# Kernel optimization log

Measured on AMD Instinct MI355X. Metric: run time of the kernel, lower is better.

The kernel has to match this reference:

```python
import jax, jax.numpy as jnp
import numpy as np

B, S, E, H = 2, 2048, 1024, 16
D = E // H  # head_dim = 64


def setup_inputs() -> dict:
    key = jax.random.key(0)
    k1, k2, k3 = jax.random.split(key, 3)
    scale = 0.02  # GPT-2 init scale
    return {
        "hidden_states": jax.random.normal(k1, (B, S, E), dtype=jnp.float32),
        "c_attn_w": jax.random.normal(k2, (E, 3 * E), dtype=jnp.float32) * scale,
        "c_attn_b": jnp.zeros((3 * E,), dtype=jnp.float32),
        "c_proj_w": jax.random.normal(k3, (E, E), dtype=jnp.float32) * scale,
        "c_proj_b": jnp.zeros((E,), dtype=jnp.float32),
    }


def reference(hidden_states, c_attn_w, c_attn_b, c_proj_w, c_proj_b):
    # Conv1D: x @ W + b  -> qkv [B, S, 3E]
    qkv = hidden_states @ c_attn_w + c_attn_b
    q, k, v = jnp.split(qkv, 3, axis=-1)

    # split heads -> [B, H, S, D]
    def split_heads(t):
        return t.reshape(B, S, H, D).transpose(0, 2, 1, 3)

    q, k, v = split_heads(q), split_heads(k), split_heads(v)

    # naive full attention: QK^T / sqrt(D) -> softmax -> @ V
    attn_weights = jnp.einsum("bhqd,bhkd->bhqk", q, k) / jnp.sqrt(
        jnp.asarray(D, dtype=q.dtype)
    )
    attn_weights = jax.nn.softmax(attn_weights, axis=-1)
    attn_output = jnp.einsum("bhqk,bhkd->bhqd", attn_weights, v)

    # merge heads -> [B, S, E], then output projection
    attn_output = attn_output.transpose(0, 2, 1, 3).reshape(B, S, E)
    attn_output = attn_output @ c_proj_w + c_proj_b
    return attn_output
```

## Files before the change

kernel.cpp:

```cpp
#include <hip/hip_runtime.h>

#define SEQ 2048
#define EMB 1024
#define KDIM 1024
#define CF 0.180336880111113f

typedef __attribute__((ext_vector_type(8))) short short8_t;
typedef __attribute__((ext_vector_type(4))) float floatx4;
typedef __attribute__((ext_vector_type(4))) unsigned short ushort4_t;
typedef __attribute__((ext_vector_type(4))) unsigned int uivec4;

#define GLOAD16(gp, lp)                                                        \
  __builtin_amdgcn_global_load_lds(                                            \
      (const __attribute__((address_space(1))) void*)(gp),                     \
      (__attribute__((address_space(3))) void*)(lp), 16, 0, 0)

#define WGBAR()                                   \
  do {                                            \
    __asm__ __volatile__("" ::: "memory");        \
    __builtin_amdgcn_s_barrier();                 \
    __asm__ __volatile__("" ::: "memory");        \
  } while (0)

static __device__ __forceinline__ unsigned short f2bf(float x) {
  unsigned int u = __float_as_uint(x);
  return (unsigned short)((u + 0x7fffu + ((u >> 16) & 1u)) >> 16);
}

static __device__ __forceinline__ short8_t mk_pb(unsigned int a, unsigned int b,
                                                 unsigned int c, unsigned int d) {
  uivec4 t;
  t[0] = a; t[1] = b; t[2] = c; t[3] = d;
  return __builtin_bit_cast(short8_t, t);
}

static __device__ __forceinline__ unsigned int pack_bf(float p0, float p1) {
  return __builtin_amdgcn_perm(__float_as_uint(p1), __float_as_uint(p0),
                               0x07060302u);
}

static __device__ __forceinline__ void tconv_tile(
    const float* __restrict__ W, unsigned short* __restrict__ T, int N, int K,
    int n0, int k0, int tid) {
  __shared__ float Tl[64][65];
  const int lx = tid & 15, ly = tid >> 4;
#pragma unroll
  for (int u = 0; u < 4; ++u) {
    int r = u * 16 + ly;
    float4 v = *(const float4*)&W[(size_t)(k0 + r) * N + n0 + lx * 4];
    Tl[r][lx * 4 + 0] = v.x;
    Tl[r][lx * 4 + 1] = v.y;
    Tl[r][lx * 4 + 2] = v.z;
    Tl[r][lx * 4 + 3] = v.w;
  }
  __syncthreads();
#pragma unroll
  for (int u = 0; u < 4; ++u) {
    int n = u * 16 + ly;
    ushort4_t h;
#pragma unroll
    for (int v = 0; v < 4; ++v) h[v] = f2bf(Tl[lx * 4 + v][n]);
    *(ushort4_t*)&T[(size_t)(n0 + n) * K + k0 + lx * 4] = h;
  }
}

__global__ __launch_bounds__(256) void prep(
    const float* __restrict__ hs, const float* __restrict__ caw,
    const float* __restrict__ cpw, unsigned short* __restrict__ hsb,
    unsigned short* __restrict__ w1t, unsigned short* __restrict__ w2t) {
  const int bid = blockIdx.x, tid = threadIdx.x;
  if (bid < 4096) {
    const int i = bid * 256 + tid;
    float4 v = *(const float4*)&hs[(size_t)i * 4];
    ushort4_t h = {f2bf(v.x), f2bf(v.y), f2bf(v.z), f2bf(v.w)};
    *(ushort4_t*)&hsb[(size_t)i * 4] = h;
  } else if (bid < 4864) {
    const int idx = bid - 4096;
    tconv_tile(caw, w1t, 3 * EMB, EMB, (idx % 48) * 64, (idx / 48) * 64, tid);
  } else {
    const int idx = bid - 4864;
    tconv_tile(cpw, w2t, EMB, EMB, (idx % 16) * 64, (idx / 16) * 64, tid);
  }
}

template <int MODE, int BN>
__global__ __launch_bounds__(256) void gemm_pl(
    const unsigned short* __restrict__ Ag, const unsigned short* __restrict__ Bg,
    const float* __restrict__ bias, float* __restrict__ outF,
    unsigned short* __restrict__ qk, unsigned short* __restrict__ vt) {
  __shared__ __attribute__((aligned(16))) unsigned short Ah[3][128 * 32];
  __shared__ __attribute__((aligned(16))) unsigned short Bh[3][BN * 32];
  const int NJ = BN / 32;

  const int tid = threadIdx.x;
  const int w = tid >> 6, lane = tid & 63;
  const int quad = lane >> 4, c = lane & 15;

  int bm, bn;
  {
    const int L = blockIdx.x, x = L & 7, g = L >> 3;
    if (MODE == 0) {
      bm = ((x & 1) * 16 + (g & 15)) * 128;
      bn = ((x >> 1) * 6 + (g >> 4)) * 128;
    } else {
      bm = ((x & 3) * 8 + (g & 7)) * 128;
      bn = ((x >> 2) * 8 + (g >> 3)) * 64;
    }
  }
  const int wm = (w >> 1) * 64, wn = (w & 1) * (BN / 2);

  const unsigned short* gsrc = (w < 2) ? Ag : Bg;
  const int lbo = (w < 2) ? (w & 1) * 64 * 32 : (w & 1) * (BN / 2) * 32;
  const int rbase = (w < 2) ? (bm + (w & 1) * 64) : (bn + (w & 1) * (BN / 2));
  const int nloads = (w < 2) ? 4 : (BN / 32);
  const int srow = lane >> 2;
  const int sblk = (lane & 3) ^ ((lane >> 3) & 3);
  const char* gp0 = (const char*)(gsrc + (size_t)(rbase + srow) * KDIM) + sblk * 16;

  floatx4 acc[4][NJ];
  const floatx4 z = {0.f, 0.f, 0.f, 0.f};
#pragma unroll
  for (int i = 0; i < 4; ++i)
#pragma unroll
    for (int j = 0; j < NJ; ++j) acc[i][j] = z;

  const int sw = (c >> 1) & 3;

#define STAGE_G(buf, kt)                                                       \
  do {                                                                         \
    unsigned short* ld = ((w < 2) ? Ah[buf] : Bh[buf]) + lbo;                  \
    const char* gp = gp0 + (size_t)(kt) * 64;                                  \
    for (int i_ = 0; i_ < nloads; ++i_)                                        \
      GLOAD16(gp + (size_t)i_ * 16 * (KDIM * 2), &ld[i_ * 512]);               \
  } while (0)

  STAGE_G(0, 0);
  STAGE_G(1, 1);

  for (int t = 0; t < 32; ++t) {
    if (BN == 128 || w < 2) {
      __asm__ __volatile__("s_waitcnt vmcnt(4)" ::: "memory");
    } else {
      __asm__ __volatile__("s_waitcnt vmcnt(2)" ::: "memory");
    }
    WGBAR();
    STAGE_G((t + 2) % 3, (t + 2) & 31);
    const unsigned short* Ac = Ah[t % 3];
    const unsigned short* Bc = Bh[t % 3];

    const int oct = (quad ^ sw) * 8;
    short8_t a[4], b[NJ];
#pragma unroll
    for (int i = 0; i < 4; ++i)
      a[i] = *(const short8_t*)&Ac[(wm + 16 * i + c) * 32 + oct];
#pragma unroll
    for (int j = 0; j < NJ; ++j)
      b[j] = *(const short8_t*)&Bc[(wn + 16 * j + c) * 32 + oct];
#pragma unroll
    for (int i = 0; i < 4; ++i)
#pragma unroll
      for (int j = 0; j < NJ; ++j)
        acc[i][j] = __builtin_amdgcn_mfma_f32_16x16x32_bf16(b[j], a[i], acc[i][j], 0, 0, 0);
  }
#undef STAGE_G

  __asm__ __volatile__("s_waitcnt vmcnt(0)" ::: "memory");

#pragma unroll
  for (int i = 0; i < 4; ++i) {
    const int row = bm + wm + 16 * i + c;
#pragma unroll
    for (int j = 0; j < NJ; ++j) {
      const int col0 = bn + wn + 16 * j + quad * 4;
      floatx4 v = acc[i][j] + *(const floatx4*)&bias[col0];
      if (MODE == 0) {
        if (col0 < 1024) v = v * CF;
        if (col0 < 2048) {
          ushort4_t pk = {f2bf(v[0]), f2bf(v[1]), f2bf(v[2]), f2bf(v[3])};
          *(ushort4_t*)&qk[(size_t)row * 2048 + col0] = pk;
        } else {
          const int c2 = col0 - 2048, hh = c2 >> 6, d0 = c2 & 63;
          const int bb = row >> 11, s = row & 2047;
          const int j = s & 63;
          const int lam = (j & 0x20) | ((j & 0x0C) << 1) | ((j & 0x10) >> 2) | (j & 3);
          const int sp = (s & ~63) | lam;
          unsigned short* vb = &vt[((size_t)(bb * 16 + hh) * 64 + d0) * 2048 + sp];
          vb[0 * 2048] = f2bf(v[0]);
          vb[1 * 2048] = f2bf(v[1]);
          vb[2 * 2048] = f2bf(v[2]);
          vb[3 * 2048] = f2bf(v[3]);
        }
      } else {
        *(floatx4*)&outF[(size_t)row * 1024 + col0] = v;
      }
    }
  }
}

static __device__ __forceinline__ void stage_kv(
    int w, int srow, int sblkg, const unsigned short* __restrict__ gK,
    const unsigned short* __restrict__ gV, unsigned short* Kbuf,
    unsigned short* Vbuf, int jt) {
  if (w < 2) {
    const unsigned short* g0 = gK + (size_t)(jt * 64 + w * 32 + srow) * 2048 + sblkg * 8;
    unsigned short* l0 = &Kbuf[(w * 32) * 64];
#pragma unroll
    for (int i = 0; i < 4; ++i) GLOAD16(g0 + (size_t)i * 8 * 2048, &l0[i * 512]);
  } else {
    const unsigned short* g0 = gV + (size_t)((w - 2) * 32 + srow) * 2048 + jt * 64 + sblkg * 8;
    unsigned short* l0 = &Vbuf[((w - 2) * 32) * 64];
#pragma unroll
    for (int i = 0; i < 4; ++i) GLOAD16(g0 + (size_t)i * 8 * 2048, &l0[i * 512]);
  }
}

__global__ __launch_bounds__(256, 4) void attn8(
    const unsigned short* __restrict__ qk, const unsigned short* __restrict__ vt,
    unsigned short* __restrict__ ao) {
  __shared__ __attribute__((aligned(16))) unsigned short SMEM[4 * 4096];
  unsigned short* Ksb = SMEM;
  unsigned short* Vsb = SMEM + 2 * 4096;

  const int tid = threadIdx.x;
  const int w = tid >> 6, lane = tid & 63, quad = lane >> 4, c = lane & 15;
  const int qh = w >> 1, kh = w & 1;
  const int L = blockIdx.x, x = L & 7, g = L >> 3;
  const int hb = x * 4 + (g >> 5);
  const int h = hb & 15, b = hb >> 4;
  const int q0 = (g & 31) * 64;
  const int rk = c & 7;

  short8_t qf[2][2];
  {
    const size_t rb = (size_t)b * SEQ + q0 + qh * 32;
#pragma unroll
    for (int mi = 0; mi < 2; ++mi) {
      const size_t qr = (rb + mi * 16 + c) * 2048 + h * 64 + quad * 8;
      qf[mi][0] = *(const short8_t*)&qk[qr];
      qf[mi][1] = *(const short8_t*)&qk[qr + 32];
    }
  }
  __asm__ __volatile__("s_waitcnt vmcnt(0)" ::: "memory");

  floatx4 O[2][4], Osum[2];
  const floatx4 z = {0.f, 0.f, 0.f, 0.f};
#pragma unroll
  for (int mi = 0; mi < 2; ++mi) {
    Osum[mi] = z;
#pragma unroll
    for (int dg = 0; dg < 4; ++dg) O[mi][dg] = z;
  }
  short8_t ones;
#pragma unroll
  for (int e = 0; e < 8; ++e) ones[e] = (short)0x3F80;

  const int srow = lane >> 3;
  const int sblkg = (lane & 7) ^ srow;
  const unsigned short* gK = qk + (size_t)b * SEQ * 2048 + 1024 + h * 64;
  const unsigned short* gV = vt + (size_t)(b * 16 + h) * 64 * 2048;

  stage_kv(w, srow, sblkg, gK, gV, Ksb, Vsb, 0);

  for (int t = 0; t < 32; ++t) {
    __asm__ __volatile__("s_waitcnt vmcnt(0)" ::: "memory");
    WGBAR();
    if (t < 31)
      stage_kv(w, srow, sblkg, gK, gV, Ksb + ((t + 1) & 1) * 4096,
               Vsb + ((t + 1) & 1) * 4096, t + 1);
    const unsigned short* Kc = Ksb + (t & 1) * 4096;
    const unsigned short* Vc = Vsb + (t & 1) * 4096;

    floatx4 S[2][2];
#pragma unroll
    for (int mi = 0; mi < 2; ++mi)
#pragma unroll
      for (int jg = 0; jg < 2; ++jg) S[mi][jg] = z;
#pragma unroll
    for (int kd = 0; kd < 2; ++kd) {
      const int oct = ((4 * kd + quad) ^ rk) * 8;
#pragma unroll
      for (int jg = 0; jg < 2; ++jg) {
        short8_t kf = *(const short8_t*)&Kc[((kh * 2 + jg) * 16 + c) * 64 + oct];
#pragma unroll
        for (int mi = 0; mi < 2; ++mi)
          S[mi][jg] = __builtin_amdgcn_mfma_f32_16x16x32_bf16(kf, qf[mi][kd], S[mi][jg], 0, 0, 0);
      }
    }

    unsigned int pw[2][2][2];
#pragma unroll
    for (int mi = 0; mi < 2; ++mi)
#pragma unroll
      for (int jg = 0; jg < 2; ++jg) {
        float p0 = __builtin_amdgcn_exp2f(S[mi][jg][0]);
        float p1 = __builtin_amdgcn_exp2f(S[mi][jg][1]);
        float p2 = __builtin_amdgcn_exp2f(S[mi][jg][2]);
        float p3 = __builtin_amdgcn_exp2f(S[mi][jg][3]);
        pw[mi][jg][0] = pack_bf(p0, p1);
        pw[mi][jg][1] = pack_bf(p2, p3);
      }

    const int octv = ((4 * kh + quad) ^ rk) * 8;
    short8_t pb[2];
#pragma unroll
    for (int mi = 0; mi < 2; ++mi) {
      pb[mi] = mk_pb(pw[mi][0][0], pw[mi][0][1], pw[mi][1][0], pw[mi][1][1]);
      Osum[mi] = __builtin_amdgcn_mfma_f32_16x16x32_bf16(ones, pb[mi], Osum[mi], 0, 0, 0);
    }
#pragma unroll
    for (int dg = 0; dg < 4; ++dg) {
      short8_t vf = *(const short8_t*)&Vc[(dg * 16 + c) * 64 + octv];
#pragma unroll
      for (int mi = 0; mi < 2; ++mi)
        O[mi][dg] = __builtin_amdgcn_mfma_f32_16x16x32_bf16(vf, pb[mi], O[mi][dg], 0, 0, 0);
    }
  }

  __asm__ __volatile__("s_waitcnt vmcnt(0)" ::: "memory");
  WGBAR();

  float* Of = (float*)SMEM;
  float* Ss = (float*)((char*)SMEM + 17408);
  if (kh == 1) {
#pragma unroll
    for (int mi = 0; mi < 2; ++mi) {
      const int row = mi * 16 + c;
      float* orow = &Of[(qh * 32 + row) * 68];
#pragma unroll
      for (int dg = 0; dg < 4; ++dg)
        *(floatx4*)&orow[dg * 16 + quad * 4] = O[mi][dg];
      if (quad == 0) Ss[qh * 32 + row] = Osum[mi][0];
    }
  }
  WGBAR();
  if (kh == 0) {
#pragma unroll
    for (int mi = 0; mi < 2; ++mi) {
      const int row = mi * 16 + c;
      const float inv = 1.0f / (Osum[mi][0] + Ss[qh * 32 + row]);
      const float* orow = &Of[(qh * 32 + row) * 68];
      const size_t grow = (size_t)b * SEQ + q0 + qh * 32 + row;
#pragma unroll
      for (int dg = 0; dg < 4; ++dg) {
        floatx4 o = O[mi][dg] + *(const floatx4*)&orow[dg * 16 + quad * 4];
        ushort4_t ov = {f2bf(o[0] * inv), f2bf(o[1] * inv),
                        f2bf(o[2] * inv), f2bf(o[3] * inv)};
        *(ushort4_t*)&ao[grow * EMB + h * 64 + dg * 16 + quad * 4] = ov;
      }
    }
  }
}

extern "C" void kernel_launch(void* const* d_in, const int* in_sizes, int n_in,
                              void* d_out, int out_size, void* d_ws, size_t ws_size,
                              hipStream_t stream) {
  const float* hs = (const float*)d_in[0];
  const float* c_attn_w = (const float*)d_in[1];
  const float* c_attn_b = (const float*)d_in[2];
  const float* c_proj_w = (const float*)d_in[3];
  const float* c_proj_b = (const float*)d_in[4];
  float* out = (float*)d_out;

  char* ws = (char*)d_ws;
  unsigned short* hsb = (unsigned short*)(ws + 0);
  unsigned short* qk  = (unsigned short*)(ws + 8388608);
  unsigned short* vt  = (unsigned short*)(ws + 25165824);
  unsigned short* aob = (unsigned short*)(ws + 33554432);
  unsigned short* w1t = (unsigned short*)(ws + 41943040);
  unsigned short* w2t = (unsigned short*)(ws + 48234496);

  prep<<<5120, 256, 0, stream>>>(hs, c_attn_w, c_proj_w, hsb, w1t, w2t);
  gemm_pl<0, 128><<<768, 256, 0, stream>>>(hsb, w1t, c_attn_b, nullptr, qk, vt);
  attn8<<<1024, 256, 0, stream>>>(qk, vt, aob);
  gemm_pl<2, 64><<<512, 256, 0, stream>>>(aob, w2t, c_proj_b, out, nullptr, nullptr);
}
```

Baseline: 176.9 us.

## Software-pipeline PV matmul one tile behind QK with triple-buffered V

Restructures the attention loop so the P·V and rowsum MFMAs for tile t-1 run after the QK^T MFMAs for tile t, which hides the exp/pack latency behind independent matrix work. V moves to a triple-buffered shared-memory ring, growing LDS to 40KB, so the previous tile's V stays valid while the next tile is staged. It also raises wave priority around the MFMA section with s_setprio. This adds register pressure from carrying pbPrev across iterations and needs an epilogue to drain the last tile.

```diff
diff --git a/kernel.cpp b/kernel.cpp
--- a/kernel.cpp
+++ b/kernel.cpp
@@ -214,10 +214,10 @@
   }
 }
 
-__global__ __launch_bounds__(256, 4) void attn8(
+__global__ __launch_bounds__(256, 4) void attn9(
     const unsigned short* __restrict__ qk, const unsigned short* __restrict__ vt,
     unsigned short* __restrict__ ao) {
-  __shared__ __attribute__((aligned(16))) unsigned short SMEM[4 * 4096];
+  __shared__ __attribute__((aligned(16))) unsigned short SMEM[5 * 4096];
   unsigned short* Ksb = SMEM;
   unsigned short* Vsb = SMEM + 2 * 4096;
 
@@ -259,6 +259,9 @@
   const unsigned short* gK = qk + (size_t)b * SEQ * 2048 + 1024 + h * 64;
   const unsigned short* gV = vt + (size_t)(b * 16 + h) * 64 * 2048;
 
+  const int octv = ((4 * kh + quad) ^ rk) * 8;
+  short8_t pbPrev[2];
+
   stage_kv(w, srow, sblkg, gK, gV, Ksb, Vsb, 0);
 
   for (int t = 0; t < 32; ++t) {
@@ -266,10 +269,10 @@
     WGBAR();
     if (t < 31)
       stage_kv(w, srow, sblkg, gK, gV, Ksb + ((t + 1) & 1) * 4096,
-               Vsb + ((t + 1) & 1) * 4096, t + 1);
+               Vsb + ((t + 1) % 3) * 4096, t + 1);
     const unsigned short* Kc = Ksb + (t & 1) * 4096;
-    const unsigned short* Vc = Vsb + (t & 1) * 4096;
-
+
+    __builtin_amdgcn_s_setprio(1);
     floatx4 S[2][2];
 #pragma unroll
     for (int mi = 0; mi < 2; ++mi)
@@ -287,36 +290,51 @@
       }
     }
 
-    unsigned int pw[2][2][2];
-#pragma unroll
-    for (int mi = 0; mi < 2; ++mi)
+    if (t != 0) {
+      const unsigned short* Vp = Vsb + ((t + 2) % 3) * 4096;
+#pragma unroll
+      for (int mi = 0; mi < 2; ++mi)
+        Osum[mi] = __builtin_amdgcn_mfma_f32_16x16x32_bf16(ones, pbPrev[mi], Osum[mi], 0, 0, 0);
+#pragma unroll
+      for (int dg = 0; dg < 4; ++dg) {
+        short8_t vf = *(const short8_t*)&Vp[(dg * 16 + c) * 64 + octv];
+#pragma unroll
+        for (int mi = 0; mi < 2; ++mi)
+          O[mi][dg] = __builtin_amdgcn_mfma_f32_16x16x32_bf16(vf, pbPrev[mi], O[mi][dg], 0, 0, 0);
+      }
+    }
+    __builtin_amdgcn_s_setprio(0);
+
+#pragma unroll
+    for (int mi = 0; mi < 2; ++mi) {
+      unsigned int pw[2][2];
 #pragma unroll
       for (int jg = 0; jg < 2; ++jg) {
         float p0 = __builtin_amdgcn_exp2f(S[mi][jg][0]);
         float p1 = __builtin_amdgcn_exp2f(S[mi][jg][1]);
         float p2 = __builtin_amdgcn_exp2f(S[mi][jg][2]);
         float p3 = __builtin_amdgcn_exp2f(S[mi][jg][3]);
-        pw[mi][jg][0] = pack_bf(p0, p1);
-        pw[mi][jg][1] = pack_bf(p2, p3);
-      }
-
-    const int octv = ((4 * kh + quad) ^ rk) * 8;
-    short8_t pb[2];
-#pragma unroll
-    for (int mi = 0; mi < 2; ++mi) {
-      pb[mi] = mk_pb(pw[mi][0][0], pw[mi][0][1], pw[mi][1][0], pw[mi][1][1]);
-      Osum[mi] = __builtin_amdgcn_mfma_f32_16x16x32_bf16(ones, pb[mi], Osum[mi], 0, 0, 0);
-    }
+        pw[jg][0] = pack_bf(p0, p1);
+        pw[jg][1] = pack_bf(p2, p3);
+      }
+      pbPrev[mi] = mk_pb(pw[0][0], pw[0][1], pw[1][0], pw[1][1]);
+    }
+  }
+
+  {
+    const unsigned short* Vp = Vsb + (31 % 3) * 4096;
+#pragma unroll
+    for (int mi = 0; mi < 2; ++mi)
+      Osum[mi] = __builtin_amdgcn_mfma_f32_16x16x32_bf16(ones, pbPrev[mi], Osum[mi], 0, 0, 0);
 #pragma unroll
     for (int dg = 0; dg < 4; ++dg) {
-      short8_t vf = *(const short8_t*)&Vc[(dg * 16 + c) * 64 + octv];
+      short8_t vf = *(const short8_t*)&Vp[(dg * 16 + c) * 64 + octv];
 #pragma unroll
       for (int mi = 0; mi < 2; ++mi)
-        O[mi][dg] = __builtin_amdgcn_mfma_f32_16x16x32_bf16(vf, pb[mi], O[mi][dg], 0, 0, 0);
-    }
-  }
-
-  __asm__ __volatile__("s_waitcnt vmcnt(0)" ::: "memory");
+        O[mi][dg] = __builtin_amdgcn_mfma_f32_16x16x32_bf16(vf, pbPrev[mi], O[mi][dg], 0, 0, 0);
+    }
+  }
+
   WGBAR();
 
   float* Of = (float*)SMEM;
@@ -371,6 +389,6 @@
 
   prep<<<5120, 256, 0, stream>>>(hs, c_attn_w, c_proj_w, hsb, w1t, w2t);
   gemm_pl<0, 128><<<768, 256, 0, stream>>>(hsb, w1t, c_attn_b, nullptr, qk, vt);
-  attn8<<<1024, 256, 0, stream>>>(qk, vt, aob);
+  attn9<<<1024, 256, 0, stream>>>(qk, vt, aob);
   gemm_pl<2, 64><<<512, 256, 0, stream>>>(aob, w2t, c_proj_b, out, nullptr, nullptr);
 }
```

Measured after the change: 181.9 us. +2.8%, slower.
